# Kernel tuning notes

Hardware: AMD Instinct MI355X
Metric: run time of the kernel (lower is better)

## Reference

```python
import jax, jax.numpy as jnp
import numpy as np

B, T, IN = 64, 512, 128
N_E, N_I, OUT = 2048, 512, 3
P_CONN, G, W_SCALE = 0.1, 4.0, 0.1
DT = 1.0
TAU_MEM_E_INV = 1.0 / 20.0
TAU_MEM_I_INV = 1.0 / 10.0
TAU_SYN_INV = 1.0 / 5.0
V_TH, V_RESET, V_LEAK = 1.0, 0.0, 0.0


def _sparse_w(k, n_post, n_pre, scale):
    k1, k2 = jax.random.split(k)
    W = jax.random.normal(k1, (n_post, n_pre)) * (scale / np.sqrt(n_pre * P_CONN))
    mask = jax.random.uniform(k2, (n_post, n_pre)) < P_CONN
    return (W * mask).astype(jnp.float32)


def setup_inputs() -> dict:
    key = jax.random.key(0)
    ks = jax.random.split(key, 10)
    x = jax.random.normal(ks[0], (B, T, IN), dtype=jnp.float32)
    W_ee = _sparse_w(ks[1], N_E, N_E, W_SCALE)
    W_ie = _sparse_w(ks[2], N_I, N_E, W_SCALE)
    W_ei = _sparse_w(ks[3], N_E, N_I, W_SCALE * G)
    W_ii = _sparse_w(ks[4], N_I, N_I, W_SCALE * G)
    W_e_in = jax.random.normal(ks[5], (N_E, IN), dtype=jnp.float32) * 0.1
    W_i_in = jax.random.normal(ks[6], (N_I, IN), dtype=jnp.float32) * 0.1
    lim = 1.0 / np.sqrt(N_E)
    readout_w = jax.random.uniform(ks[7], (OUT, N_E), minval=-lim, maxval=lim, dtype=jnp.float32)
    readout_b = jax.random.uniform(ks[8], (OUT,), minval=-lim, maxval=lim, dtype=jnp.float32)
    return {"x": x, "W_ee": W_ee, "W_ie": W_ie, "W_ei": W_ei, "W_ii": W_ii,
            "W_e_in": W_e_in, "W_i_in": W_i_in,
            "readout_w": readout_w, "readout_b": readout_b}


def _heaviside(x):
    return (x > 0).astype(x.dtype)


def _lif_step(v, i, I_in, tau_mem_inv):
    # norse-style LIF update (dt folded in)
    v_dec = v + DT * tau_mem_inv * ((V_LEAK - v) + i)
    i_dec = i * (1.0 - DT * TAU_SYN_INV)
    z = _heaviside(v_dec - V_TH)
    v_new = (1.0 - z) * v_dec + z * V_RESET
    i_new = i_dec + I_in
    return z, v_new, i_new


def reference(x, W_ee, W_ie, W_ei, W_ii, W_e_in, W_i_in, readout_w, readout_b):
    # relu-masked recurrent weights (computed once, as F.relu(W) each step is constant)
    Wee, Wie = jax.nn.relu(W_ee), jax.nn.relu(W_ie)
    Wei, Wii = jax.nn.relu(W_ei), jax.nn.relu(W_ii)

    def step(carry, x_t):
        v_e, i_e, v_i, i_i, s_e, s_i = carry
        I_e = x_t @ W_e_in.T + s_e @ Wee.T - s_i @ Wei.T
        I_i = x_t @ W_i_in.T + s_e @ Wie.T - s_i @ Wii.T
        z_e, v_e, i_e = _lif_step(v_e, i_e, I_e, TAU_MEM_E_INV)
        z_i, v_i, i_i = _lif_step(v_i, i_i, I_i, TAU_MEM_I_INV)
        return (v_e, i_e, v_i, i_i, z_e, z_i), z_e

    zeros_e = jnp.zeros((B, N_E), x.dtype)
    zeros_i = jnp.zeros((B, N_I), x.dtype)
    init = (zeros_e, zeros_e, zeros_i, zeros_i, zeros_e, zeros_i)
    _, spikes_e = jax.lax.scan(step, init, jnp.swapaxes(x, 0, 1))  # [T,B,N_E]
    rates_e = spikes_e.mean(axis=0)  # readout_mode='rate'
    return rates_e @ readout_w.T + readout_b
```

## Files before the change

### kernel.cpp

```cpp
#include <hip/hip_runtime.h>
#include <hip/hip_fp16.h>
#include <cstdint>
#include <cstddef>

#define N_E 2048
#define N_I 512
#define N_TOT 2560
#define BATCH 64
#define TSTEPS 512
#define INDIM 128
#define GD 32

typedef float f32x4 __attribute__((ext_vector_type(4)));

#define TS 64
__global__ __launch_bounds__(256) void build_wd_kernel(
    const float* __restrict__ Wee, const float* __restrict__ Wie,
    const float* __restrict__ Wei, const float* __restrict__ Wii,
    __half* __restrict__ Wd)
{
    __shared__ float tile[TS][TS + 1];
    int P0 = blockIdx.x * TS;
    int Q0 = blockIdx.y * TS;
    int tx = threadIdx.x & 63, ty = threadIdx.x >> 6;

    const float* W; int ldw, po_off, pr_off; float sign;
    bool preE = (P0 < N_E), postE = (Q0 < N_E);
    if (postE && preE)        { W = Wee; ldw = N_E; po_off = 0;   pr_off = 0;   sign =  1.f; }
    else if (!postE && preE)  { W = Wie; ldw = N_E; po_off = N_E; pr_off = 0;   sign =  1.f; }
    else if (postE && !preE)  { W = Wei; ldw = N_I; po_off = 0;   pr_off = N_E; sign = -1.f; }
    else                      { W = Wii; ldw = N_I; po_off = N_E; pr_off = N_E; sign = -1.f; }

    for (int r = ty; r < TS; r += 4) {
        int post = Q0 + r, pre = P0 + tx;
        float v = W[(size_t)(post - po_off) * ldw + (pre - pr_off)];
        tile[r][tx] = (v > 0.f) ? sign * v : 0.f;
    }
    __syncthreads();
    for (int r = ty; r < TS; r += 4) {
        int pre = P0 + r, post = Q0 + tx;
        Wd[(size_t)pre * N_TOT + post] = __float2half(tile[tx][r]);
    }
}

#define PBM 128
#define PBN 64
#define PBK 32
__global__ __launch_bounds__(256) void proj_kernel(
    const float* __restrict__ x, const float* __restrict__ We, const float* __restrict__ Wi,
    float* __restrict__ out, int t0)
{
    __shared__ __align__(16) float As[PBK][132];
    __shared__ __align__(16) float Bs[PBK][68];
    int tid = threadIdx.x;
    int bx = blockIdx.x, by = blockIdx.y;
    int tx = tid & 15, ty = tid >> 4;
    float acc[8][4];
#pragma unroll
    for (int i = 0; i < 8; ++i)
#pragma unroll
        for (int j = 0; j < 4; ++j) acc[i][j] = 0.0f;

    for (int kb = 0; kb < INDIM; kb += PBK) {
#pragma unroll
        for (int it = 0; it < 4; ++it) {
            int idx = it * 256 + tid;
            int kq = idx & 7, ml = idx >> 3;
            int m = by * PBM + ml;
            int b = m & 63, tl = m >> 6;
            const float* arow = x + ((size_t)b * TSTEPS + (size_t)(t0 + tl)) * INDIM;
            float4 v = *(const float4*)(arow + kb + kq * 4);
            As[kq * 4 + 0][ml] = v.x; As[kq * 4 + 1][ml] = v.y;
            As[kq * 4 + 2][ml] = v.z; As[kq * 4 + 3][ml] = v.w;
        }
#pragma unroll
        for (int it = 0; it < 2; ++it) {
            int idx = it * 256 + tid;
            int kq = idx & 7, nl = idx >> 3;
            int n = bx * PBN + nl;
            const float* brow = (n < N_E) ? (We + (size_t)n * INDIM)
                                          : (Wi + (size_t)(n - N_E) * INDIM);
            float4 v = *(const float4*)(brow + kb + kq * 4);
            Bs[kq * 4 + 0][nl] = v.x; Bs[kq * 4 + 1][nl] = v.y;
            Bs[kq * 4 + 2][nl] = v.z; Bs[kq * 4 + 3][nl] = v.w;
        }
        __syncthreads();
#pragma unroll
        for (int k = 0; k < PBK; ++k) {
            float4 a0 = *(const float4*)&As[k][ty * 8];
            float4 a1 = *(const float4*)&As[k][ty * 8 + 4];
            float4 b0 = *(const float4*)&Bs[k][tx * 4];
            float a[8] = {a0.x, a0.y, a0.z, a0.w, a1.x, a1.y, a1.z, a1.w};
            float bb[4] = {b0.x, b0.y, b0.z, b0.w};
#pragma unroll
            for (int i = 0; i < 8; ++i)
#pragma unroll
                for (int j = 0; j < 4; ++j)
                    acc[i][j] = fmaf(a[i], bb[j], acc[i][j]);
        }
        __syncthreads();
    }
#pragma unroll
    for (int i = 0; i < 8; ++i) {
        int m = by * PBM + ty * 8 + i;
        f32x4 o = { acc[i][0], acc[i][1], acc[i][2], acc[i][3] };
        __builtin_nontemporal_store(o, (f32x4*)(out + (size_t)m * N_TOT + bx * PBN + tx * 4));
    }
}

__device__ __forceinline__ float inline_proj(const float* __restrict__ x,
                                             const float* __restrict__ We_in,
                                             const float* __restrict__ Wi_in,
                                             int b, int t, int n)
{
    const float* xr = x + ((size_t)b * TSTEPS + (size_t)t) * INDIM;
    const float* wr = (n < N_E) ? (We_in + (size_t)n * INDIM)
                                : (Wi_in + (size_t)(n - N_E) * INDIM);
    float a = 0.f;
#pragma unroll
    for (int k = 0; k < INDIM; k += 4) {
        float4 w = *(const float4*)(wr + k);
        float4 xv = *(const float4*)(xr + k);
        a = fmaf(w.x, xv.x, a); a = fmaf(w.y, xv.y, a);
        a = fmaf(w.z, xv.z, a); a = fmaf(w.w, xv.w, a);
    }
    return a;
}

__global__ __launch_bounds__(640) void sim_kernel(
    const float* __restrict__ i_inp,
    const float* __restrict__ x, const float* __restrict__ We_in, const float* __restrict__ Wi_in,
    const __half* __restrict__ Wd,
    float* __restrict__ gv, float* __restrict__ gi, unsigned* __restrict__ g_cnt,
    int* __restrict__ g_list, int* __restrict__ g_nspk,
    int t0, int tc, int first)
{
    __shared__ int list_s[2][N_TOT];
    __shared__ int nspk_s[2];

    int b = blockIdx.x, tid = threadIdx.x, lane = tid & 63;
    int p0 = tid * 4;
    bool isE = (tid < 512);
    float tm = isE ? 0.05f : 0.1f;

    float v0, v1, v2, v3, c0, c1, c2, c3;
    unsigned n0c = 0u, n1c = 0u, n2c = 0u, n3c = 0u;
    if (first) {
        v0 = v1 = v2 = v3 = 0.f; c0 = c1 = c2 = c3 = 0.f;
        if (tid == 0) nspk_s[0] = 0;
    } else {
        float4 vv = *(const float4*)(gv + (size_t)b * N_TOT + p0);
        float4 cc = *(const float4*)(gi + (size_t)b * N_TOT + p0);
        v0 = vv.x; v1 = vv.y; v2 = vv.z; v3 = vv.w;
        c0 = cc.x; c1 = cc.y; c2 = cc.z; c3 = cc.w;
        if (isE) {
            uint4 q = *(const uint4*)(g_cnt + (size_t)b * N_E + p0);
            n0c = q.x; n1c = q.y; n2c = q.z; n3c = q.w;
        }
        if (tid == 0) nspk_s[0] = g_nspk[b];
    }
    __syncthreads();
    if (!first) {
        int n0 = nspk_s[0];
        for (int s = tid; s < n0; s += 640) list_s[0][s] = g_list[(size_t)b * N_TOT + s];
    }
    __syncthreads();

    const unsigned short* Wdu = (const unsigned short*)Wd;

    f32x4 pf = { 0.f, 0.f, 0.f, 0.f };
    if (i_inp)
        pf = __builtin_nontemporal_load((const f32x4*)(i_inp + (size_t)b * N_TOT + p0));

    for (int tl = 0; tl < tc; ++tl) {
        int cur = tl & 1, nxt = cur ^ 1;
        if (tid == 0) nspk_s[nxt] = 0;

        float I0, I1, I2, I3;
        f32x4 pfn = { 0.f, 0.f, 0.f, 0.f };
        if (i_inp) {
            I0 = pf.x; I1 = pf.y; I2 = pf.z; I3 = pf.w;
            if (tl + 1 < tc)
                pfn = __builtin_nontemporal_load(
                    (const f32x4*)(i_inp + ((size_t)(tl + 1) * BATCH + b) * N_TOT + p0));
        } else {
            const float* xr = x + ((size_t)b * TSTEPS + (size_t)(t0 + tl)) * INDIM;
            const float* w0 = isE ? (We_in + (size_t)p0 * INDIM)
                                  : (Wi_in + (size_t)(p0 - N_E) * INDIM);
            I0 = I1 = I2 = I3 = 0.f;
            for (int k = 0; k < INDIM; ++k) {
                float xv = xr[k];
                I0 = fmaf(w0[k], xv, I0);
                I1 = fmaf(w0[INDIM + k], xv, I1);
                I2 = fmaf(w0[2 * INDIM + k], xv, I2);
                I3 = fmaf(w0[3 * INDIM + k], xv, I3);
            }
        }

        int ns = nspk_s[cur];
        const int* lst = list_s[cur];
        for (int s0 = 0; s0 < ns; s0 += GD) {
            int take = ns - s0; if (take > GD) take = GD;
            ushort4 w[GD];
#pragma unroll
            for (int k = 0; k < GD; ++k) {
                if (k < take) {
                    int j = lst[s0 + k];
                    w[k] = *(const ushort4*)(Wdu + (size_t)j * N_TOT + p0);
                }
            }
#pragma unroll
            for (int k = 0; k < GD; ++k) {
                if (k < take) {
                    I0 += __half2float(__ushort_as_half(w[k].x));
                    I1 += __half2float(__ushort_as_half(w[k].y));
                    I2 += __half2float(__ushort_as_half(w[k].z));
                    I3 += __half2float(__ushort_as_half(w[k].w));
                }
            }
        }

        float vd0 = v0 + tm * (c0 - v0); bool z0 = vd0 > 1.0f; v0 = z0 ? 0.f : vd0; c0 = 0.8f * c0 + I0;
        float vd1 = v1 + tm * (c1 - v1); bool z1 = vd1 > 1.0f; v1 = z1 ? 0.f : vd1; c1 = 0.8f * c1 + I1;
        float vd2 = v2 + tm * (c2 - v2); bool z2 = vd2 > 1.0f; v2 = z2 ? 0.f : vd2; c2 = 0.8f * c2 + I2;
        float vd3 = v3 + tm * (c3 - v3); bool z3 = vd3 > 1.0f; v3 = z3 ? 0.f : vd3; c3 = 0.8f * c3 + I3;
        if (isE) { n0c += z0; n1c += z1; n2c += z2; n3c += z3; }

        __syncthreads();

        unsigned long long m0 = __ballot(z0), m1 = __ballot(z1);
        unsigned long long m2 = __ballot(z2), m3 = __ballot(z3);
        int w0c = __popcll(m0), w1c = __popcll(m1), w2c = __popcll(m2), w3c = __popcll(m3);
        int tot = w0c + w1c + w2c + w3c;
        if (tot) {
            int base = 0;
            if (lane == 0) base = atomicAdd(&nspk_s[nxt], tot);
            base = __shfl(base, 0);
            unsigned long long pre = (1ull << lane) - 1ull;
            if (z0) list_s[nxt][base + __popcll(m0 & pre)] = p0;
            if (z1) list_s[nxt][base + w0c + __popcll(m1 & pre)] = p0 + 1;
            if (z2) list_s[nxt][base + w0c + w1c + __popcll(m2 & pre)] = p0 + 2;
            if (z3) list_s[nxt][base + w0c + w1c + w2c + __popcll(m3 & pre)] = p0 + 3;
        }
        __syncthreads();
        pf = pfn;
    }

    *(float4*)(gv + (size_t)b * N_TOT + p0) = make_float4(v0, v1, v2, v3);
    *(float4*)(gi + (size_t)b * N_TOT + p0) = make_float4(c0, c1, c2, c3);
    if (isE) *(uint4*)(g_cnt + (size_t)b * N_E + p0) = make_uint4(n0c, n1c, n2c, n3c);
    int fin = tc & 1;
    if (tid == 0) g_nspk[b] = nspk_s[fin];
    for (int s = tid; s < nspk_s[fin]; s += 640) g_list[(size_t)b * N_TOT + s] = list_s[fin][s];
}

__global__ __launch_bounds__(256) void readout_kernel(
    const unsigned* __restrict__ g_cnt,
    const float* __restrict__ rw, const float* __restrict__ rb, float* __restrict__ out)
{
    int b = blockIdx.x, tid = threadIdx.x;
    float a0 = 0.f, a1 = 0.f, a2 = 0.f;
    for (int n = tid; n < N_E; n += 256) {
        float c = (float)g_cnt[(size_t)b * N_E + n];
        a0 = fmaf(c, rw[n], a0);
        a1 = fmaf(c, rw[N_E + n], a1);
        a2 = fmaf(c, rw[2 * N_E + n], a2);
    }
#pragma unroll
    for (int off = 32; off > 0; off >>= 1) {
        a0 += __shfl_down(a0, off);
        a1 += __shfl_down(a1, off);
        a2 += __shfl_down(a2, off);
    }
    __shared__ float part[3][4];
    int wid = tid >> 6, lane = tid & 63;
    if (lane == 0) { part[0][wid] = a0; part[1][wid] = a1; part[2][wid] = a2; }
    __syncthreads();
    if (tid == 0) {
        float s0 = part[0][0] + part[0][1] + part[0][2] + part[0][3];
        float s1 = part[1][0] + part[1][1] + part[1][2] + part[1][3];
        float s2 = part[2][0] + part[2][1] + part[2][2] + part[2][3];
        const float inv = 1.0f / 512.0f;
        out[b * 3 + 0] = fmaf(s0, inv, rb[0]);
        out[b * 3 + 1] = fmaf(s1, inv, rb[1]);
        out[b * 3 + 2] = fmaf(s2, inv, rb[2]);
    }
}

extern "C" void kernel_launch(void* const* d_in, const int* in_sizes, int n_in,
                              void* d_out, int out_size, void* d_ws, size_t ws_size,
                              hipStream_t stream)
{
    const float* x     = (const float*)d_in[0];
    const float* Wee   = (const float*)d_in[1];
    const float* Wie   = (const float*)d_in[2];
    const float* Wei   = (const float*)d_in[3];
    const float* Wii   = (const float*)d_in[4];
    const float* We_in = (const float*)d_in[5];
    const float* Wi_in = (const float*)d_in[6];
    const float* rw    = (const float*)d_in[7];
    const float* rb    = (const float*)d_in[8];
    float* out = (float*)d_out;
    char* ws = (char*)d_ws;

    size_t off = 0;
    auto alloc = [&](size_t bytes) {
        size_t o = off;
        off = (off + bytes + 255) & ~(size_t)255;
        return o;
    };
    size_t o_wd    = alloc((size_t)N_TOT * N_TOT * 2);
    size_t o_gv    = alloc((size_t)BATCH * N_TOT * 4);
    size_t o_gi    = alloc((size_t)BATCH * N_TOT * 4);
    size_t o_gcnt  = alloc((size_t)BATCH * N_E * 4);
    size_t o_glist = alloc((size_t)BATCH * N_TOT * 4);
    size_t o_gnspk = alloc((size_t)BATCH * 4);
    size_t o_iinp  = off;

    int tc = 0;
    if (ws_size > o_iinp) {
        size_t avail = ws_size - o_iinp;
        tc = TSTEPS;
        while (tc >= 2 && (size_t)tc * BATCH * N_TOT * 4 > avail) tc >>= 1;
        if (tc < 2) tc = 0;
    }

    __half*   p_wd    = (__half*)(ws + o_wd);
    float*    p_gv    = (float*)(ws + o_gv);
    float*    p_gi    = (float*)(ws + o_gi);
    unsigned* p_gcnt  = (unsigned*)(ws + o_gcnt);
    int*      p_glist = (int*)(ws + o_glist);
    int*      p_gnspk = (int*)(ws + o_gnspk);
    float*    p_iinp  = (float*)(ws + o_iinp);

    dim3 wg(N_TOT / TS, N_TOT / TS);
    build_wd_kernel<<<wg, 256, 0, stream>>>(Wee, Wie, Wei, Wii, p_wd);

    if (tc >= 2) {
        for (int t0 = 0; t0 < TSTEPS; t0 += tc) {
            dim3 pg(N_TOT / PBN, (tc * BATCH) / PBM);
            proj_kernel<<<pg, 256, 0, stream>>>(x, We_in, Wi_in, p_iinp, t0);
            sim_kernel<<<BATCH, 640, 0, stream>>>(
                p_iinp, x, We_in, Wi_in, p_wd,
                p_gv, p_gi, p_gcnt, p_glist, p_gnspk,
                t0, tc, (t0 == 0) ? 1 : 0);
        }
    } else {
        sim_kernel<<<BATCH, 640, 0, stream>>>(
            nullptr, x, We_in, Wi_in, p_wd,
            p_gv, p_gi, p_gcnt, p_glist, p_gnspk,
            0, TSTEPS, 1);
    }

    readout_kernel<<<BATCH, 256, 0, stream>>>(p_gcnt, rw, rb, out);
}
```

Measured before the change: 2.590 ms.

## Compress recurrent weight rows into bitmask plus packed fp16 values

Adds a preprocessing kernel that turns each dense fp16 row of the combined recurrent matrix into a 1280-byte record. Each record holds a 32-bit occupancy mask per 32 columns, prefix counts, and the packed nonzero values. The simulation kernel reads the mask and prefix count for each spiking presynaptic neuron, then gathers only the nonzero weights it needs, and the gather batch size drops from 32 to 16. The aim is to cut the per-spike weight traffic and the working set so it stays cache resident. In exchange, each accumulation now needs a dependent second load and popcount arithmetic, and rows with more than 400 nonzeros are silently truncated.

Measured after the change: 9.393 ms. 263% more time.

```diff
diff --git a/kernel.cpp b/kernel.cpp
--- a/kernel.cpp
+++ b/kernel.cpp
@@ -9,7 +9,8 @@
 #define BATCH 64
 #define TSTEPS 512
 #define INDIM 128
-#define GD 32
+#define GD 16
+#define ROWB 1280
 
 typedef float f32x4 __attribute__((ext_vector_type(4)));
 
@@ -40,6 +41,39 @@
     for (int r = ty; r < TS; r += 4) {
         int pre = P0 + r, post = Q0 + tx;
         Wd[(size_t)pre * N_TOT + post] = __float2half(tile[tx][r]);
+    }
+}
+
+__global__ __launch_bounds__(128) void compress_kernel(
+    const __half* __restrict__ Wd, char* __restrict__ sp)
+{
+    __shared__ unsigned short cnt_s[80];
+    __shared__ unsigned short cum_s[80];
+    int j = blockIdx.x, t = threadIdx.x;
+    const unsigned short* row = (const unsigned short*)(Wd + (size_t)j * N_TOT);
+    unsigned mask = 0;
+    if (t < 80) {
+        int cnt = 0;
+        for (int b = 0; b < 32; ++b) {
+            unsigned short h = row[t * 32 + b];
+            if (h & 0x7FFF) { mask |= (1u << b); ++cnt; }
+        }
+        cnt_s[t] = (unsigned short)cnt;
+    }
+    __syncthreads();
+    if (t == 0) {
+        unsigned a = 0;
+        for (int w = 0; w < 80; ++w) { cum_s[w] = (unsigned short)a; a += cnt_s[w]; }
+    }
+    __syncthreads();
+    char* rb = sp + (size_t)j * ROWB;
+    if (t < 80) {
+        ((unsigned*)rb)[t] = mask;
+        ((unsigned short*)(rb + 320))[t] = cum_s[t];
+        unsigned short* vals = (unsigned short*)(rb + 480);
+        int o = cum_s[t];
+        for (int b = 0; b < 32; ++b)
+            if ((mask >> b) & 1u) { if (o < 400) vals[o] = row[t * 32 + b]; ++o; }
     }
 }
 
@@ -130,7 +164,7 @@
 __global__ __launch_bounds__(640) void sim_kernel(
     const float* __restrict__ i_inp,
     const float* __restrict__ x, const float* __restrict__ We_in, const float* __restrict__ Wi_in,
-    const __half* __restrict__ Wd,
+    const char* __restrict__ sp,
     float* __restrict__ gv, float* __restrict__ gi, unsigned* __restrict__ g_cnt,
     int* __restrict__ g_list, int* __restrict__ g_nspk,
     int t0, int tc, int first)
@@ -142,6 +176,8 @@
     int p0 = tid * 4;
     bool isE = (tid < 512);
     float tm = isE ? 0.05f : 0.1f;
+    int word = tid >> 3;
+    int sh = (tid & 7) * 4;
 
     float v0, v1, v2, v3, c0, c1, c2, c3;
     unsigned n0c = 0u, n1c = 0u, n2c = 0u, n3c = 0u;
@@ -165,8 +201,6 @@
         for (int s = tid; s < n0; s += 640) list_s[0][s] = g_list[(size_t)b * N_TOT + s];
     }
     __syncthreads();
-
-    const unsigned short* Wdu = (const unsigned short*)Wd;
 
     f32x4 pf = { 0.f, 0.f, 0.f, 0.f };
     if (i_inp)
@@ -201,21 +235,32 @@
         const int* lst = list_s[cur];
         for (int s0 = 0; s0 < ns; s0 += GD) {
             int take = ns - s0; if (take > GD) take = GD;
-            ushort4 w[GD];
+            unsigned off[GD]; unsigned bw[GD]; unsigned short cum[GD];
 #pragma unroll
             for (int k = 0; k < GD; ++k) {
                 if (k < take) {
-                    int j = lst[s0 + k];
-                    w[k] = *(const ushort4*)(Wdu + (size_t)j * N_TOT + p0);
+                    off[k] = (unsigned)lst[s0 + k] * (unsigned)ROWB;
+                    bw[k] = *(const unsigned*)(sp + off[k] + (size_t)word * 4);
+                    cum[k] = *(const unsigned short*)(sp + off[k] + 320 + (size_t)word * 2);
                 }
             }
 #pragma unroll
             for (int k = 0; k < GD; ++k) {
                 if (k < take) {
-                    I0 += __half2float(__ushort_as_half(w[k].x));
-                    I1 += __half2float(__ushort_as_half(w[k].y));
-                    I2 += __half2float(__ushort_as_half(w[k].z));
-                    I3 += __half2float(__ushort_as_half(w[k].w));
+                    unsigned nib = (bw[k] >> sh) & 0xFu;
+                    if (nib) {
+                        int idx = (int)cum[k] + __popc(bw[k] & ((1u << sh) - 1u));
+                        const unsigned short* vals =
+                            (const unsigned short*)(sp + off[k] + 480);
+                        if (nib & 1u)
+                            I0 += __half2float(__ushort_as_half(vals[idx]));
+                        if (nib & 2u)
+                            I1 += __half2float(__ushort_as_half(vals[idx + __popc(nib & 1u)]));
+                        if (nib & 4u)
+                            I2 += __half2float(__ushort_as_half(vals[idx + __popc(nib & 3u)]));
+                        if (nib & 8u)
+                            I3 += __half2float(__ushort_as_half(vals[idx + __popc(nib & 7u)]));
+                    }
                 }
             }
         }
@@ -310,6 +355,7 @@
         return o;
     };
     size_t o_wd    = alloc((size_t)N_TOT * N_TOT * 2);
+    size_t o_sp    = alloc((size_t)N_TOT * ROWB);
     size_t o_gv    = alloc((size_t)BATCH * N_TOT * 4);
     size_t o_gi    = alloc((size_t)BATCH * N_TOT * 4);
     size_t o_gcnt  = alloc((size_t)BATCH * N_E * 4);
@@ -326,6 +372,7 @@
     }
 
     __half*   p_wd    = (__half*)(ws + o_wd);
+    char*     p_sp    = ws + o_sp;
     float*    p_gv    = (float*)(ws + o_gv);
     float*    p_gi    = (float*)(ws + o_gi);
     unsigned* p_gcnt  = (unsigned*)(ws + o_gcnt);
@@ -335,19 +382,20 @@
 
     dim3 wg(N_TOT / TS, N_TOT / TS);
     build_wd_kernel<<<wg, 256, 0, stream>>>(Wee, Wie, Wei, Wii, p_wd);
+    compress_kernel<<<N_TOT, 128, 0, stream>>>(p_wd, p_sp);
 
     if (tc >= 2) {
         for (int t0 = 0; t0 < TSTEPS; t0 += tc) {
             dim3 pg(N_TOT / PBN, (tc * BATCH) / PBM);
             proj_kernel<<<pg, 256, 0, stream>>>(x, We_in, Wi_in, p_iinp, t0);
             sim_kernel<<<BATCH, 640, 0, stream>>>(
-                p_iinp, x, We_in, Wi_in, p_wd,
+                p_iinp, x, We_in, Wi_in, p_sp,
                 p_gv, p_gi, p_gcnt, p_glist, p_gnspk,
                 t0, tc, (t0 == 0) ? 1 : 0);
         }
     } else {
         sim_kernel<<<BATCH, 640, 0, stream>>>(
-            nullptr, x, We_in, Wi_in, p_wd,
+            nullptr, x, We_in, Wi_in, p_sp,
             p_gv, p_gi, p_gcnt, p_glist, p_gnspk,
             0, TSTEPS, 1);
     }
```
